# Performance work log

Hardware: AMD Instinct MI355X
Metric: run time of the kernel (lower is better)

The kernel has to match this reference:

```python
import jax, jax.numpy as jnp
import numpy as np

KERNEL_MUL = 2.0
KERNEL_NUM = 5
FIX_SIGMA = None


def setup_inputs() -> dict:
    key = jax.random.key(0)
    k1, k2 = jax.random.split(key)
    source = jax.random.normal(k1, (4096, 64), dtype=jnp.float32)
    target = jax.random.normal(k2, (4096, 64), dtype=jnp.float32)
    return {"source": source, "target": target}


def reference(source, target):
    batch_size = source.shape[0]
    total = jnp.concatenate([source, target], axis=0)  # [2N, D]
    n_samples = total.shape[0]
    sq = jnp.sum(total * total, axis=1)  # [2N]
    L2 = sq[:, None] + sq[None, :] - 2.0 * (total @ total.T)  # [2N, 2N]
    if FIX_SIGMA:
        bandwidth = jnp.asarray(FIX_SIGMA, dtype=L2.dtype)
    else:
        # torch uses L2_distance.data -> detached; no grad through bandwidth
        bandwidth = jax.lax.stop_gradient(jnp.sum(L2)) / (n_samples ** 2 - n_samples)
    bandwidth = bandwidth / (KERNEL_MUL ** (KERNEL_NUM // 2))
    kernels = jnp.zeros_like(L2)
    for i in range(KERNEL_NUM):  # small fixed loop over bandwidths
        kernels = kernels + jnp.exp(-L2 / (bandwidth * (KERNEL_MUL ** i)))
    XX = kernels[:batch_size, :batch_size]
    YY = kernels[batch_size:, batch_size:]
    XY = kernels[:batch_size, batch_size:]
    YX = kernels[batch_size:, :batch_size]
    return jnp.mean(XX + YY - XY - YX)
```

## Files before the change

kernel.cpp:

```cpp
#include <hip/hip_runtime.h>
#include <math.h>

#define N_TOTAL 8192
#define BATCH   4096
#define DIMS    64
#define P1_BLOCKS 256
#define SEG     8
#define NSEG    16
#define NPART   2048


#if defined(__has_builtin)
#if __has_builtin(__builtin_amdgcn_exp2f)
#define EXP2F(x) __builtin_amdgcn_exp2f(x)
#endif
#endif
#ifndef EXP2F
#define EXP2F(x) exp2f(x)
#endif

typedef __attribute__((ext_vector_type(8))) short bf16x8;
typedef __attribute__((ext_vector_type(4))) float f32x4;
typedef __attribute__((ext_vector_type(2))) float f32x2;
typedef __attribute__((ext_vector_type(4))) short s16x4;

__device__ inline short f2bf_rn(float x) {
    unsigned u = __float_as_uint(x);
    unsigned r = (u + 0x7fffu + ((u >> 16) & 1u)) >> 16;
    return (short)r;
}

__global__ __launch_bounds__(256) void pass1_kernel(const float* __restrict__ src,
                                                    const float* __restrict__ tgt,
                                                    double* __restrict__ sqpart,
                                                    double* __restrict__ colpart,
                                                    float* __restrict__ sqbuf,
                                                    short* __restrict__ Xh) {
    __shared__ double cred[4][64];
    __shared__ double sred[4];
    const int lane = threadIdx.x & 63;
    const int wv = threadIdx.x >> 6;
    const int sub = lane >> 4;
    const int k4 = (lane & 15) << 2;
    const int gw = blockIdx.x * 4 + wv;
    const int numWaves = P1_BLOCKS * 4;

    double colacc[4] = {0.0, 0.0, 0.0, 0.0};
    double sqacc = 0.0;

    for (int g = gw; g < N_TOTAL / 4; g += numWaves) {
        int r = g * 4 + sub;
        const float* row = (r < BATCH) ? (src + (size_t)r * DIMS)
                                       : (tgt + (size_t)(r - BATCH) * DIMS);
        float4 v = *(const float4*)(row + k4);
        float xs[4] = {v.x, v.y, v.z, v.w};
        s16x4 h;
        float ssum = 0.f;
        #pragma unroll
        for (int i = 0; i < 4; ++i) {
            h[i] = f2bf_rn(xs[i]);
            colacc[i] += (double)xs[i];
            ssum = fmaf(xs[i], xs[i], ssum);
        }
        *(s16x4*)(Xh + (size_t)r * DIMS + k4) = h;
        ssum += __shfl_xor(ssum, 1, 64);
        ssum += __shfl_xor(ssum, 2, 64);
        ssum += __shfl_xor(ssum, 4, 64);
        ssum += __shfl_xor(ssum, 8, 64);
        if ((lane & 15) == 0) { sqbuf[r] = ssum; sqacc += (double)ssum; }
    }
    #pragma unroll
    for (int i = 0; i < 4; ++i) {
        colacc[i] += __shfl_xor(colacc[i], 16, 64);
        colacc[i] += __shfl_xor(colacc[i], 32, 64);
    }
    sqacc += __shfl_xor(sqacc, 16, 64);
    sqacc += __shfl_xor(sqacc, 32, 64);
    if (lane < 16) {
        #pragma unroll
        for (int i = 0; i < 4; ++i) cred[wv][lane * 4 + i] = colacc[i];
    }
    if (lane == 0) sred[wv] = sqacc;
    __syncthreads();
    if (wv == 0) {
        double c = (cred[0][lane] + cred[1][lane]) + (cred[2][lane] + cred[3][lane]);
        colpart[(size_t)blockIdx.x * 64 + lane] = c;
        if (lane == 0)
            sqpart[blockIdx.x] = (sred[0] + sred[1]) + (sred[2] + sred[3]);
    }
}

__global__ __launch_bounds__(256) void scale_kernel(const double* __restrict__ sqpart,
                                                    const double* __restrict__ colpart,
                                                    float* __restrict__ csp) {
    __shared__ double cred[4][64];
    __shared__ double sred[4];
    const int t = threadIdx.x;
    const int lane = t & 63, w = t >> 6;

    double colacc = 0.0;
    #pragma unroll 4
    for (int b = w; b < P1_BLOCKS; b += 4)
        colacc += colpart[(size_t)b * 64 + lane];
    cred[w][lane] = colacc;

    double sacc = sqpart[t];
    #pragma unroll
    for (int off = 32; off > 0; off >>= 1) sacc += __shfl_xor(sacc, off, 64);
    if (lane == 0) sred[w] = sacc;
    __syncthreads();

    if (w == 0) {
        double colsum = (cred[0][lane] + cred[1][lane])
                      + (cred[2][lane] + cred[3][lane]);
        double vv = colsum * colsum;
        #pragma unroll
        for (int off = 32; off > 0; off >>= 1) vv += __shfl_xor(vv, off, 64);
        if (lane == 0) {
            double sq = (sred[0] + sred[1]) + (sred[2] + sred[3]);
            const double n = (double)N_TOTAL;
            double bw0 = (2.0 * n * sq - 2.0 * vv) / (n * n - n) * 0.25;
            csp[0] = (float)(-1.0 / (bw0 * 0.6931471805599453 * 16.0));
        }
    }
}

__global__ __launch_bounds__(512) void pass2_kernel(const short* __restrict__ Xh,
                                                    const float* __restrict__ sqbuf,
                                                    const float* __restrict__ csp,
                                                    float* __restrict__ partials) {
    const int bc = blockIdx.x;
    const int r0 = blockIdx.y * SEG;
    const int pidx = blockIdx.y * 128 + bc;
    const int t = threadIdx.x;
    if (r0 > bc) {
        if (t == 0) partials[pidx] = 0.f;
        return;
    }
    const int r1 = (bc < r0 + SEG - 1) ? bc : r0 + SEG - 1;

    __shared__ __align__(16) short Bh[64][72];
    __shared__ float s_wred[8];

    const int lane = t & 63, w = t >> 6;
    const int strip = w & 3, ts = w >> 2;
    const int quad = lane >> 4, lrow = lane & 15;

    {
        int row = t >> 3;
        int c8 = (t & 7) << 3;
        size_t gsrc = (size_t)(bc * 64 + row) * DIMS + c8;
        *(s16x4*)&Bh[row][c8]     = *(const s16x4*)(Xh + gsrc);
        *(s16x4*)&Bh[row][c8 + 4] = *(const s16x4*)(Xh + gsrc + 4);
    }
    const float cs = csp[0];
    const float c2 = -2.f * cs;
    const f32x2 c2v = (f32x2){c2, c2};
    f32x2 sbj[4];
    #pragma unroll
    for (int j = 0; j < 4; ++j) {
        float s = sqbuf[bc * 64 + j * 16 + lrow] * cs;
        sbj[j] = (f32x2){s, s};
    }
    __syncthreads();

    const size_t aoff = (size_t)(strip * 16 + lrow) * DIMS + quad * 8;

    float facc = 0.f;

    for (int r = r0 + ts; r <= r1; r += 2) {
        const size_t abase = (size_t)r * 64 * DIMS + aoff;
        bf16x8 ah0 = *(const bf16x8*)(Xh + abase);
        bf16x8 ah1 = *(const bf16x8*)(Xh + abase + 32);
        float4 csa = *(const float4*)(sqbuf + r * 64 + strip * 16 + quad * 4);

        f32x4 acc[4];
        #pragma unroll
        for (int j = 0; j < 4; ++j) acc[j] = (f32x4){0.f, 0.f, 0.f, 0.f};
        #pragma unroll
        for (int j = 0; j < 4; ++j) {
            const int brow = j * 16 + lrow;
            const int bcol = quad * 8;
            bf16x8 bh0 = *(const bf16x8*)&Bh[brow][bcol];
            bf16x8 bh1 = *(const bf16x8*)&Bh[brow][bcol + 32];
            acc[j] = __builtin_amdgcn_mfma_f32_16x16x32_bf16(ah0, bh0, acc[j], 0, 0, 0);
            acc[j] = __builtin_amdgcn_mfma_f32_16x16x32_bf16(ah1, bh1, acc[j], 0, 0, 0);
        }

        const f32x2 sa01 = (f32x2){csa.x * cs, csa.y * cs};
        const f32x2 sa23 = (f32x2){csa.z * cs, csa.w * cs};
        f32x2 lsum2 = (f32x2){0.f, 0.f};
        #pragma unroll
        for (int j = 0; j < 4; ++j) {
            f32x2 a01 = (f32x2){acc[j][0], acc[j][1]};
            f32x2 a23 = (f32x2){acc[j][2], acc[j][3]};
            f32x2 t01 = a01 * c2v + (sa01 + sbj[j]);
            f32x2 t23 = a23 * c2v + (sa23 + sbj[j]);
            f32x2 e4a = (f32x2){EXP2F(t01[0]), EXP2F(t01[1])};
            f32x2 e4b = (f32x2){EXP2F(t23[0]), EXP2F(t23[1])};
            f32x2 e3a = e4a * e4a, e3b = e4b * e4b;
            f32x2 e2a = e3a * e3a, e2b = e3b * e3b;
            f32x2 e1a = e2a * e2a, e1b = e2b * e2b;
            f32x2 e0a = e1a * e1a, e0b = e1b * e1b;
            lsum2 += ((e0a + e1a) + (e2a + e3a)) + e4a;
            lsum2 += ((e0b + e1b) + (e2b + e3b)) + e4b;
        }
        float lsum = lsum2[0] + lsum2[1];
        float sgn = ((r < 64) == (bc < 64)) ? 1.f : -1.f;
        float wt  = (r == bc) ? 1.f : 2.f;
        facc = fmaf(lsum, sgn * wt, facc);
    }

    #pragma unroll
    for (int off = 32; off > 0; off >>= 1) facc += __shfl_xor(facc, off, 64);
    if (lane == 0) s_wred[w] = facc;
    __syncthreads();
    if (t == 0)
        partials[pidx] = ((s_wred[0] + s_wred[1]) + (s_wred[2] + s_wred[3]))
                       + ((s_wred[4] + s_wred[5]) + (s_wred[6] + s_wred[7]));
}

__global__ __launch_bounds__(256) void finalize_kernel(const float* __restrict__ partials,
                                                       float* __restrict__ out) {
    __shared__ double s_red[4];
    const int t = threadIdx.x;
    const int lane = t & 63, w = t >> 6;
    double acc = 0.0;
    #pragma unroll
    for (int i = 0; i < NPART / 256; ++i)
        acc += (double)partials[t + 256 * i];
    #pragma unroll
    for (int off = 32; off > 0; off >>= 1) acc += __shfl_xor(acc, off, 64);
    if (lane == 0) s_red[w] = acc;
    __syncthreads();
    if (t == 0) {
        double g = (s_red[0] + s_red[1]) + (s_red[2] + s_red[3]);
        out[0] = (float)(g / ((double)BATCH * (double)BATCH));
    }
}

extern "C" void kernel_launch(void* const* d_in, const int* in_sizes, int n_in,
                              void* d_out, int out_size, void* d_ws, size_t ws_size,
                              hipStream_t stream) {
    const float* src = (const float*)d_in[0];
    const float* tgt = (const float*)d_in[1];
    char* ws = (char*)d_ws;
    double* sqpart  = (double*)ws;
    double* colpart = (double*)(ws + 2048);
    float*  csp     = (float*)(ws + 133120);
    float*  parts   = (float*)(ws + 133632);
    float*  sqbuf   = (float*)(ws + 141824);
    short*  Xh      = (short*)(ws + 262144);


    pass1_kernel<<<P1_BLOCKS, 256, 0, stream>>>(src, tgt, sqpart, colpart,
                                                sqbuf, Xh);
    scale_kernel<<<1, 256, 0, stream>>>(sqpart, colpart, csp);

    dim3 grid(128, NSEG);
    pass2_kernel<<<grid, 512, 0, stream>>>(Xh, sqbuf, csp, parts);

    finalize_kernel<<<1, 256, 0, stream>>>(parts, (float*)d_out);
}
```

Baseline: 84.50 us.

## Fuse finalize into pass2 via last-block atomic counter and prefetch A tiles

Removes the separate finalize kernel launch by having each pass2 block bump an atomic counter, with the last block reducing all partials and writing the output. The counter is reset inside scale_kernel. The pass2 inner loop also now software-prefetches the next row tile's A fragments and squared norms while the current tile is processed. This saves one launch gap and hides some global-load latency, at the cost of a threadfence and atomic per block and some extra registers.

```diff
diff --git a/kernel.cpp b/kernel.cpp
--- a/kernel.cpp
+++ b/kernel.cpp
@@ -92,11 +92,13 @@
 
 __global__ __launch_bounds__(256) void scale_kernel(const double* __restrict__ sqpart,
                                                     const double* __restrict__ colpart,
-                                                    float* __restrict__ csp) {
+                                                    float* __restrict__ csp,
+                                                    int* __restrict__ cnt2) {
     __shared__ double cred[4][64];
     __shared__ double sred[4];
     const int t = threadIdx.x;
     const int lane = t & 63, w = t >> 6;
+    if (t == 0) *cnt2 = 0;
 
     double colacc = 0.0;
     #pragma unroll 4
@@ -128,114 +130,132 @@
 __global__ __launch_bounds__(512) void pass2_kernel(const short* __restrict__ Xh,
                                                     const float* __restrict__ sqbuf,
                                                     const float* __restrict__ csp,
-                                                    float* __restrict__ partials) {
+                                                    float* __restrict__ partials,
+                                                    int* __restrict__ cnt2,
+                                                    float* __restrict__ out) {
     const int bc = blockIdx.x;
     const int r0 = blockIdx.y * SEG;
     const int pidx = blockIdx.y * 128 + bc;
     const int t = threadIdx.x;
-    if (r0 > bc) {
-        if (t == 0) partials[pidx] = 0.f;
-        return;
-    }
-    const int r1 = (bc < r0 + SEG - 1) ? bc : r0 + SEG - 1;
+    const int lane = t & 63, w = t >> 6;
+    const bool live = (r0 <= bc);
 
     __shared__ __align__(16) short Bh[64][72];
     __shared__ float s_wred[8];
-
-    const int lane = t & 63, w = t >> 6;
-    const int strip = w & 3, ts = w >> 2;
-    const int quad = lane >> 4, lrow = lane & 15;
-
-    {
-        int row = t >> 3;
-        int c8 = (t & 7) << 3;
-        size_t gsrc = (size_t)(bc * 64 + row) * DIMS + c8;
-        *(s16x4*)&Bh[row][c8]     = *(const s16x4*)(Xh + gsrc);
-        *(s16x4*)&Bh[row][c8 + 4] = *(const s16x4*)(Xh + gsrc + 4);
-    }
-    const float cs = csp[0];
-    const float c2 = -2.f * cs;
-    const f32x2 c2v = (f32x2){c2, c2};
-    f32x2 sbj[4];
-    #pragma unroll
-    for (int j = 0; j < 4; ++j) {
-        float s = sqbuf[bc * 64 + j * 16 + lrow] * cs;
-        sbj[j] = (f32x2){s, s};
-    }
+    __shared__ int s_last;
+
+    if (live) {
+        const int r1 = (bc < r0 + SEG - 1) ? bc : r0 + SEG - 1;
+        const int strip = w & 3, ts = w >> 2;
+        const int quad = lane >> 4, lrow = lane & 15;
+
+        {
+            int row = t >> 3;
+            int c8 = (t & 7) << 3;
+            size_t gsrc = (size_t)(bc * 64 + row) * DIMS + c8;
+            *(s16x4*)&Bh[row][c8]     = *(const s16x4*)(Xh + gsrc);
+            *(s16x4*)&Bh[row][c8 + 4] = *(const s16x4*)(Xh + gsrc + 4);
+        }
+        const float cs = csp[0];
+        const float c2 = -2.f * cs;
+        const f32x2 c2v = (f32x2){c2, c2};
+        f32x2 sbj[4];
+        #pragma unroll
+        for (int j = 0; j < 4; ++j) {
+            float s = sqbuf[bc * 64 + j * 16 + lrow] * cs;
+            sbj[j] = (f32x2){s, s};
+        }
+        __syncthreads();
+
+        const size_t aoff = (size_t)(strip * 16 + lrow) * DIMS + quad * 8;
+
+        const int rs = r0 + ts;
+        size_t abase = (size_t)rs * 64 * DIMS + aoff;
+        bf16x8 ah0, ah1; float4 csa;
+        if (rs <= r1) {
+            ah0 = *(const bf16x8*)(Xh + abase);
+            ah1 = *(const bf16x8*)(Xh + abase + 32);
+            csa = *(const float4*)(sqbuf + rs * 64 + strip * 16 + quad * 4);
+        }
+
+        float facc = 0.f;
+
+        for (int r = rs; r <= r1; r += 2) {
+            bf16x8 cah0 = ah0, cah1 = ah1;
+            float4 ccsa = csa;
+            int rn = (r + 2 <= r1) ? r + 2 : r;
+            size_t nbase = (size_t)rn * 64 * DIMS + aoff;
+            ah0 = *(const bf16x8*)(Xh + nbase);
+            ah1 = *(const bf16x8*)(Xh + nbase + 32);
+            csa = *(const float4*)(sqbuf + rn * 64 + strip * 16 + quad * 4);
+
+            f32x4 acc[4];
+            #pragma unroll
+            for (int j = 0; j < 4; ++j) acc[j] = (f32x4){0.f, 0.f, 0.f, 0.f};
+            #pragma unroll
+            for (int j = 0; j < 4; ++j) {
+                const int brow = j * 16 + lrow;
+                const int bcol = quad * 8;
+                bf16x8 bh0 = *(const bf16x8*)&Bh[brow][bcol];
+                bf16x8 bh1 = *(const bf16x8*)&Bh[brow][bcol + 32];
+                acc[j] = __builtin_amdgcn_mfma_f32_16x16x32_bf16(cah0, bh0, acc[j], 0, 0, 0);
+                acc[j] = __builtin_amdgcn_mfma_f32_16x16x32_bf16(cah1, bh1, acc[j], 0, 0, 0);
+            }
+
+            const f32x2 sa01 = (f32x2){ccsa.x * cs, ccsa.y * cs};
+            const f32x2 sa23 = (f32x2){ccsa.z * cs, ccsa.w * cs};
+            f32x2 lsum2 = (f32x2){0.f, 0.f};
+            #pragma unroll
+            for (int j = 0; j < 4; ++j) {
+                f32x2 a01 = (f32x2){acc[j][0], acc[j][1]};
+                f32x2 a23 = (f32x2){acc[j][2], acc[j][3]};
+                f32x2 t01 = a01 * c2v + (sa01 + sbj[j]);
+                f32x2 t23 = a23 * c2v + (sa23 + sbj[j]);
+                f32x2 e4a = (f32x2){EXP2F(t01[0]), EXP2F(t01[1])};
+                f32x2 e4b = (f32x2){EXP2F(t23[0]), EXP2F(t23[1])};
+                f32x2 e3a = e4a * e4a, e3b = e4b * e4b;
+                f32x2 e2a = e3a * e3a, e2b = e3b * e3b;
+                f32x2 e1a = e2a * e2a, e1b = e2b * e2b;
+                f32x2 e0a = e1a * e1a, e0b = e1b * e1b;
+                lsum2 += ((e0a + e1a) + (e2a + e3a)) + e4a;
+                lsum2 += ((e0b + e1b) + (e2b + e3b)) + e4b;
+            }
+            float lsum = lsum2[0] + lsum2[1];
+            float sgn = ((r < 64) == (bc < 64)) ? 1.f : -1.f;
+            float wt  = (r == bc) ? 1.f : 2.f;
+            facc = fmaf(lsum, sgn * wt, facc);
+        }
+
+        #pragma unroll
+        for (int off = 32; off > 0; off >>= 1) facc += __shfl_xor(facc, off, 64);
+        if (lane == 0) s_wred[w] = facc;
+        __syncthreads();
+        if (t == 0)
+            partials[pidx] = ((s_wred[0] + s_wred[1]) + (s_wred[2] + s_wred[3]))
+                           + ((s_wred[4] + s_wred[5]) + (s_wred[6] + s_wred[7]));
+    } else {
+        if (t == 0) partials[pidx] = 0.f;
+    }
+
+    __threadfence();
+    if (t == 0) s_last = (atomicAdd(cnt2, 1) == NPART - 1) ? 1 : 0;
     __syncthreads();
-
-    const size_t aoff = (size_t)(strip * 16 + lrow) * DIMS + quad * 8;
-
-    float facc = 0.f;
-
-    for (int r = r0 + ts; r <= r1; r += 2) {
-        const size_t abase = (size_t)r * 64 * DIMS + aoff;
-        bf16x8 ah0 = *(const bf16x8*)(Xh + abase);
-        bf16x8 ah1 = *(const bf16x8*)(Xh + abase + 32);
-        float4 csa = *(const float4*)(sqbuf + r * 64 + strip * 16 + quad * 4);
-
-        f32x4 acc[4];
-        #pragma unroll
-        for (int j = 0; j < 4; ++j) acc[j] = (f32x4){0.f, 0.f, 0.f, 0.f};
-        #pragma unroll
-        for (int j = 0; j < 4; ++j) {
-            const int brow = j * 16 + lrow;
-            const int bcol = quad * 8;
-            bf16x8 bh0 = *(const bf16x8*)&Bh[brow][bcol];
-            bf16x8 bh1 = *(const bf16x8*)&Bh[brow][bcol + 32];
-            acc[j] = __builtin_amdgcn_mfma_f32_16x16x32_bf16(ah0, bh0, acc[j], 0, 0, 0);
-            acc[j] = __builtin_amdgcn_mfma_f32_16x16x32_bf16(ah1, bh1, acc[j], 0, 0, 0);
-        }
-
-        const f32x2 sa01 = (f32x2){csa.x * cs, csa.y * cs};
-        const f32x2 sa23 = (f32x2){csa.z * cs, csa.w * cs};
-        f32x2 lsum2 = (f32x2){0.f, 0.f};
-        #pragma unroll
-        for (int j = 0; j < 4; ++j) {
-            f32x2 a01 = (f32x2){acc[j][0], acc[j][1]};
-            f32x2 a23 = (f32x2){acc[j][2], acc[j][3]};
-            f32x2 t01 = a01 * c2v + (sa01 + sbj[j]);
-            f32x2 t23 = a23 * c2v + (sa23 + sbj[j]);
-            f32x2 e4a = (f32x2){EXP2F(t01[0]), EXP2F(t01[1])};
-            f32x2 e4b = (f32x2){EXP2F(t23[0]), EXP2F(t23[1])};
-            f32x2 e3a = e4a * e4a, e3b = e4b * e4b;
-            f32x2 e2a = e3a * e3a, e2b = e3b * e3b;
-            f32x2 e1a = e2a * e2a, e1b = e2b * e2b;
-            f32x2 e0a = e1a * e1a, e0b = e1b * e1b;
-            lsum2 += ((e0a + e1a) + (e2a + e3a)) + e4a;
-            lsum2 += ((e0b + e1b) + (e2b + e3b)) + e4b;
-        }
-        float lsum = lsum2[0] + lsum2[1];
-        float sgn = ((r < 64) == (bc < 64)) ? 1.f : -1.f;
-        float wt  = (r == bc) ? 1.f : 2.f;
-        facc = fmaf(lsum, sgn * wt, facc);
-    }
-
-    #pragma unroll
-    for (int off = 32; off > 0; off >>= 1) facc += __shfl_xor(facc, off, 64);
-    if (lane == 0) s_wred[w] = facc;
-    __syncthreads();
-    if (t == 0)
-        partials[pidx] = ((s_wred[0] + s_wred[1]) + (s_wred[2] + s_wred[3]))
-                       + ((s_wred[4] + s_wred[5]) + (s_wred[6] + s_wred[7]));
-}
-
-__global__ __launch_bounds__(256) void finalize_kernel(const float* __restrict__ partials,
-                                                       float* __restrict__ out) {
-    __shared__ double s_red[4];
-    const int t = threadIdx.x;
-    const int lane = t & 63, w = t >> 6;
-    double acc = 0.0;
-    #pragma unroll
-    for (int i = 0; i < NPART / 256; ++i)
-        acc += (double)partials[t + 256 * i];
-    #pragma unroll
-    for (int off = 32; off > 0; off >>= 1) acc += __shfl_xor(acc, off, 64);
-    if (lane == 0) s_red[w] = acc;
-    __syncthreads();
-    if (t == 0) {
-        double g = (s_red[0] + s_red[1]) + (s_red[2] + s_red[3]);
-        out[0] = (float)(g / ((double)BATCH * (double)BATCH));
+    if (s_last) {
+        __threadfence();
+        double acc = 0.0;
+        #pragma unroll
+        for (int i = 0; i < NPART / 512; ++i)
+            acc += (double)atomicAdd(&partials[t + 512 * i], 0.f);
+        #pragma unroll
+        for (int off = 32; off > 0; off >>= 1) acc += __shfl_xor(acc, off, 64);
+        __shared__ double s_red[8];
+        if (lane == 0) s_red[w] = acc;
+        __syncthreads();
+        if (t == 0) {
+            double g = ((s_red[0] + s_red[1]) + (s_red[2] + s_red[3]))
+                     + ((s_red[4] + s_red[5]) + (s_red[6] + s_red[7]));
+            out[0] = (float)(g / ((double)BATCH * (double)BATCH));
+        }
     }
 }
 
@@ -248,6 +268,7 @@
     double* sqpart  = (double*)ws;
     double* colpart = (double*)(ws + 2048);
     float*  csp     = (float*)(ws + 133120);
+    int*    cnt2    = (int*)(ws + 133124);
     float*  parts   = (float*)(ws + 133632);
     float*  sqbuf   = (float*)(ws + 141824);
     short*  Xh      = (short*)(ws + 262144);
@@ -255,10 +276,9 @@
 
     pass1_kernel<<<P1_BLOCKS, 256, 0, stream>>>(src, tgt, sqpart, colpart,
                                                 sqbuf, Xh);
-    scale_kernel<<<1, 256, 0, stream>>>(sqpart, colpart, csp);
+    scale_kernel<<<1, 256, 0, stream>>>(sqpart, colpart, csp, cnt2);
 
     dim3 grid(128, NSEG);
-    pass2_kernel<<<grid, 512, 0, stream>>>(Xh, sqbuf, csp, parts);
-
-    finalize_kernel<<<1, 256, 0, stream>>>(parts, (float*)d_out);
-}
+    pass2_kernel<<<grid, 512, 0, stream>>>(Xh, sqbuf, csp, parts,
+                                           cnt2, (float*)d_out);
+}
```

Result: slower. 327.8 us (+288.0%).
